# Kernel tuning notes

Hardware: AMD Instinct MI355X
Metric: run time of the kernel (lower is better)

## Reference

```python
import jax, jax.numpy as jnp
import numpy as np
from jax import lax

B, T, D_IN, H1, H2 = 200, 500, 300, 256, 300


def _lstm(x, Wih, Whh, bih, bhh, H):
    """PyTorch-convention LSTM (gate order i,f,g,o), zero init state.
    x: [B,T,Din] -> outputs [B,T,H]."""
    b = x.shape[0]
    # Precompute input contribution for all timesteps: [B,T,4H]
    xg = jnp.einsum('bti,gi->btg', x, Wih) + bih + bhh

    def step(carry, xg_t):
        h, c = carry
        g = xg_t + h @ Whh.T  # [B,4H]
        i = jax.nn.sigmoid(g[:, :H])
        f = jax.nn.sigmoid(g[:, H:2 * H])
        gg = jnp.tanh(g[:, 2 * H:3 * H])
        o = jax.nn.sigmoid(g[:, 3 * H:])
        c = f * c + i * gg
        h = o * jnp.tanh(c)
        return (h, c), h

    init = (jnp.zeros((b, H), x.dtype), jnp.zeros((b, H), x.dtype))
    _, hs = lax.scan(step, init, jnp.swapaxes(xg, 0, 1))  # [T,B,H]
    return jnp.swapaxes(hs, 0, 1)


def _uniform(key, shape, H):
    s = 1.0 / np.sqrt(H)
    return jax.random.uniform(key, shape, jnp.float32, -s, s)


def setup_inputs() -> dict:
    key = jax.random.key(0)
    ks = jax.random.split(key, 10)
    x = jax.random.normal(ks[0], (B, T, D_IN), jnp.float32)
    lengths = jax.random.randint(ks[1], (B,), 1, T + 1, jnp.int32)
    return {
        'x': x,
        'lengths': lengths,
        'Wih1': _uniform(ks[2], (4 * H1, D_IN), H1),
        'Whh1': _uniform(ks[3], (4 * H1, H1), H1),
        'bih1': _uniform(ks[4], (4 * H1,), H1),
        'bhh1': _uniform(ks[5], (4 * H1,), H1),
        'Wih2': _uniform(ks[6], (4 * H2, H1), H2),
        'Whh2': _uniform(ks[7], (4 * H2, H2), H2),
        'bih2': _uniform(ks[8], (4 * H2,), H2),
        'bhh2': _uniform(ks[9], (4 * H2,), H2),
    }


def reference(x, lengths, Wih1, Whh1, bih1, bhh1, Wih2, Whh2, bih2, bhh2):
    # lstm1 on packed sequence == causal per-sample LSTM + zero out padding
    out1 = _lstm(x, Wih1, Whh1, bih1, bhh1, H1)  # [B,T,H1]
    mask = (jnp.arange(T)[None, :] < lengths[:, None])  # [B,T]
    out1 = out1 * mask[:, :, None].astype(out1.dtype)   # pad_packed zeros
    # vectorized "last valid timestep" gather (replaces host-sync loop)
    idx = (lengths - 1).astype(jnp.int32)[:, None, None]
    h_value = jnp.take_along_axis(out1, idx, axis=1)[:, 0, :]  # [B,H1]
    # lstm2 runs over the full padded (zeroed) sequence, as in the original
    out2 = _lstm(out1, Wih2, Whh2, bih2, bhh2, H2)  # [B,T,H2]
    return (out2, h_value)
```

## Files before the change

### kernel.cpp

```cpp
#include <hip/hip_runtime.h>
#include <math.h>

#define TSEQ 500
#define BQ   200
#define DIN  300
#define H1   256
#define H2   300
#define K1   556
#define KP   576
#define H1P  256
#define H2P  304
#define BQC  25
#define LB1  8
#define LBT  18
#define NBLK 144

#define H1SLOT (BQ*H1P)
#define H2SLOT (BQ*H2P)

#define WS_H1   0
#define WS_H2   307200
#define WS_C1   672000
#define WS_C2   876800
#define WS_FLG  1132800
#define WS_MSET 1133824

#define POISON 0xFFFFFFFFFFFFFFFFull

typedef __attribute__((ext_vector_type(8))) short short8;
typedef __attribute__((ext_vector_type(4))) float f32x4;
typedef unsigned long long u64;

__device__ __forceinline__ float sigf(float v){ return 1.0f/(1.0f+__expf(-v)); }
__device__ __forceinline__ float tanhf_(float v){
    v = fminf(15.0f, fmaxf(-15.0f, v));
    float e = __expf(2.0f*v);
    return (e-1.0f)/(e+1.0f);
}
__device__ __forceinline__ unsigned short f2bf(float f){
    unsigned int xx = __builtin_bit_cast(unsigned int, f);
    xx = (xx + 0x7FFFu + ((xx>>16)&1u)) >> 16;
    return (unsigned short)xx;
}
__device__ __forceinline__ u64 ld8_sys(const void* p){
    return __hip_atomic_load((const u64*)p, __ATOMIC_RELAXED, __HIP_MEMORY_SCOPE_SYSTEM);
}
__device__ __forceinline__ void pub8(u64* p, u64 v){
    u64 old = __hip_atomic_exchange(p, v, __ATOMIC_RELAXED, __HIP_MEMORY_SCOPE_SYSTEM);
    asm volatile("" :: "v"(old));
}

union U16B { short8 s8; u64 u[2]; unsigned short us[8]; };
union U8B  { u64 u; unsigned short us[4]; };


__global__ __launch_bounds__(512, 2)
void lstm_mfma(const float* __restrict__ x, const int* __restrict__ lengths,
               const float* __restrict__ Wih1, const float* __restrict__ Whh1,
               const float* __restrict__ bih1, const float* __restrict__ bhh1,
               const float* __restrict__ Wih2, const float* __restrict__ Whh2,
               const float* __restrict__ bih2, const float* __restrict__ bhh2,
               float* __restrict__ out, char* __restrict__ wsb,
               int it_begin, int it_end, int coop)
{
    __shared__ unsigned short Al[32*KP];
    __shared__ float gl[128*33];
    __shared__ float bias[128];
    __shared__ int lenl[32];

    const int tid = threadIdx.x;
    const int bid = blockIdx.x;
    const int mc  = bid & 7;
    const int lbi = bid >> 3;
    const bool l1 = lbi < LB1;
    const int ub  = (l1 ? lbi : lbi - LB1) * 32;
    const int Hl  = l1 ? H1 : H2;

    unsigned short* h1s = (unsigned short*)(wsb + WS_H1);
    unsigned short* h2s = (unsigned short*)(wsb + WS_H2);
    float* c1 = (float*)(wsb + WS_C1);
    float* c2 = (float*)(wsb + WS_C2);
    int* flg = (int*)(wsb + WS_FLG + mc*128);

    const int wave = tid >> 6, lane = tid & 63;
    const int fr = lane & 15, fg = lane >> 4;
    const int sw = fr & 7;

    short8 wreg[18];
    {
        const int row = wave*16 + fr;
        const int u = row >> 2, g = row & 3;
        const int unit = ub + u;
        const bool vr = unit < Hl;
        const long grow = (long)g*Hl + unit;
        #pragma unroll
        for (int ks = 0; ks < 18; ++ks){
            unsigned short v8[8];
            #pragma unroll
            for (int j = 0; j < 8; ++j){
                int k = ks*32 + fg*8 + j;
                float v = 0.0f;
                if (vr && k < K1){
                    if (l1) v = (k < H1) ? Whh1[grow*H1 + k] : Wih1[grow*DIN + (k - H1)];
                    else    v = (k < H1) ? Wih2[grow*H1 + k] : Whh2[grow*H2 + (k - H1)];
                }
                v8[j] = f2bf(v);
            }
            wreg[ks] = *(short8*)v8;
        }
    }
    if (tid < 128){
        int u = tid >> 2, g = tid & 3, unit = ub + u;
        bias[tid] = (unit < Hl)
            ? ((l1?bih1:bih2)[g*Hl+unit] + (l1?bhh1:bhh2)[g*Hl+unit]) : 0.0f;
    }
    if (tid < 32) lenl[tid] = (tid < BQC) ? lengths[mc*BQC + tid] : 0;

    const unsigned short* arow0 = &Al[fr*KP];
    const unsigned short* arow1 = &Al[(16+fr)*KP];
    const int bg_e = mc*BQC + lane;
    const int unit4 = ub + wave*4;

    float creg[4] = {0.f, 0.f, 0.f, 0.f};
    if (!coop && lane < 32){
        float* cs = l1 ? c1 : c2;
        #pragma unroll
        for (int i2 = 0; i2 < 4; ++i2) creg[i2] = cs[(unit4 + i2)*BQ + bg_e];
    }

    __syncthreads();

    for (int it = it_begin; it < it_end; ++it){
        const bool active = l1 ? (it < TSEQ) : (it >= 1);
        const int t = l1 ? it : it - 1;

        if (l1){
            if (active){
                #pragma unroll
                for (int i = 0; i < 3; ++i){
                    int e = tid + i*512;
                    if (e < 1280){
                        int bl = e/40, kcx = 32 + e - (e/40)*40;
                        U16B v; v.u[0] = 0; v.u[1] = 0;
                        if (bl < BQC && kcx <= 69){
                            int bg = mc*BQC + bl;
                            const float* xp = x + ((size_t)bg*TSEQ + t)*DIN + (kcx*8 - 256);
                            float4 f0 = *(const float4*)xp;
                            v.us[0]=f2bf(f0.x); v.us[1]=f2bf(f0.y); v.us[2]=f2bf(f0.z); v.us[3]=f2bf(f0.w);
                            if (kcx <= 68){
                                float4 f1 = *(const float4*)(xp + 4);
                                v.us[4]=f2bf(f1.x); v.us[5]=f2bf(f1.y); v.us[6]=f2bf(f1.z); v.us[7]=f2bf(f1.w);
                            }
                        }
                        *(short8*)&Al[bl*KP + ((kcx ^ (bl&7))<<3)] = v.s8;
                    }
                }
                const unsigned short* h1p = h1s + (it%3)*H1SLOT;
                const int bl0 = tid>>5, kc0 = tid&31;
                const int bl1 = bl0 + 16;
                u64 a0=0, a1=0, a2=0, a3=0;
                const u64* p0 = (const u64*)(h1p + (size_t)(mc*BQC + bl0)*H1P + kc0*8);
                const u64* p2 = (const u64*)(h1p + (size_t)(mc*BQC + bl1)*H1P + kc0*8);
                const bool n0 = bl0 < BQC, n1 = bl1 < BQC;
                if (coop){
                    if (n0){ a0 = POISON; a1 = POISON; }
                    if (n1){ a2 = POISON; a3 = POISON; }
                    bool pend = n0 | n1;
                    while (pend){
                        if (a0 == POISON) a0 = ld8_sys(p0);
                        if (a1 == POISON) a1 = ld8_sys(p0 + 1);
                        if (a2 == POISON) a2 = ld8_sys(p2);
                        if (a3 == POISON) a3 = ld8_sys(p2 + 1);
                        pend = (a0==POISON)||(a1==POISON)||(a2==POISON)||(a3==POISON);
                        if (pend) __builtin_amdgcn_s_sleep(1);
                    }
                } else {
                    if (n0){ a0 = ld8_sys(p0); a1 = ld8_sys(p0 + 1); }
                    if (n1){ a2 = ld8_sys(p2); a3 = ld8_sys(p2 + 1); }
                }
                U16B w0; w0.u[0] = a0; w0.u[1] = a1;
                U16B w1; w1.u[0] = a2; w1.u[1] = a3;
                *(short8*)&Al[bl0*KP + ((kc0 ^ (bl0&7))<<3)] = w0.s8;
                *(short8*)&Al[bl1*KP + ((kc0 ^ (bl1&7))<<3)] = w1.s8;
            }
        } else {
            if (active){
                const unsigned short* h1p = h1s + (it%3)*H1SLOT;
                const unsigned short* h2p = h2s + ((it+2)%3)*H2SLOT;
                const u64* pp[5]; bool qa[5], qb[5]; u64 va[5], vb[5];
                #pragma unroll
                for (int i = 0; i < 5; ++i){
                    const int e = tid + i*512;
                    const int bl = e/72, kc = e - (e/72)*72;
                    pp[i] = nullptr; qa[i] = false; qb[i] = false; va[i] = 0; vb[i] = 0;
                    if (e < 2304 && bl < BQC && kc < 70){
                        const int bg = mc*BQC + bl;
                        if (kc < 32){
                            if (t < lenl[bl]){
                                pp[i] = (const u64*)(h1p + (size_t)bg*H1P + kc*8);
                                qa[i] = true; qb[i] = true;
                            }
                        } else {
                            pp[i] = (const u64*)(h2p + (size_t)bg*H2P + (kc*8 - 256));
                            qa[i] = true; qb[i] = (kc < 69);
                        }
                    }
                }
                if (coop){
                    #pragma unroll
                    for (int i = 0; i < 5; ++i){ if (qa[i]) va[i] = POISON; if (qb[i]) vb[i] = POISON; }
                    bool pend = true;
                    while (pend){
                        pend = false;
                        #pragma unroll
                        for (int i = 0; i < 5; ++i){
                            if (qa[i] && va[i] == POISON){ va[i] = ld8_sys(pp[i]);     pend |= (va[i] == POISON); }
                            if (qb[i] && vb[i] == POISON){ vb[i] = ld8_sys(pp[i] + 1); pend |= (vb[i] == POISON); }
                        }
                        if (pend) __builtin_amdgcn_s_sleep(1);
                    }
                } else {
                    #pragma unroll
                    for (int i = 0; i < 5; ++i){
                        if (qa[i]) va[i] = ld8_sys(pp[i]);
                        if (qb[i]) vb[i] = ld8_sys(pp[i] + 1);
                    }
                }
                #pragma unroll
                for (int i = 0; i < 5; ++i){
                    const int e = tid + i*512;
                    if (e < 2304){
                        const int bl = e/72, kc = e - (e/72)*72;
                        U16B v; v.u[0] = va[i]; v.u[1] = vb[i];
                        *(short8*)&Al[bl*KP + ((kc ^ (bl&7))<<3)] = v.s8;
                    }
                }
            }
        }

        __syncthreads();
        if (!l1 && coop && tid == 0)
            __hip_atomic_store(&flg[lbi], it + 1, __ATOMIC_RELAXED,
                               __HIP_MEMORY_SCOPE_SYSTEM);

        if (coop && lane < BQC){
            if (l1){
                if (it + 1 < TSEQ)
                    pub8((u64*)&h1s[((it+2)%3)*H1SLOT + (size_t)bg_e*H1P + unit4], POISON);
            } else if (unit4 < H2){
                pub8((u64*)&h2s[((it+1)%3)*H2SLOT + (size_t)bg_e*H2P + unit4], POISON);
            }
        }

        if (active){
            f32x4 acc0 = {0.f,0.f,0.f,0.f}, acc1 = {0.f,0.f,0.f,0.f};
            #pragma unroll
            for (int ks = 0; ks < 18; ++ks){
                const int off = ((ks*4 + fg) ^ sw) << 3;
                short8 b0 = *(const short8*)(arow0 + off);
                short8 b1 = *(const short8*)(arow1 + off);
                acc0 = __builtin_amdgcn_mfma_f32_16x16x32_bf16(wreg[ks], b0, acc0, 0, 0, 0);
                acc1 = __builtin_amdgcn_mfma_f32_16x16x32_bf16(wreg[ks], b1, acc1, 0, 0, 0);
            }
            const int gr = wave*16 + fg*4;
            #pragma unroll
            for (int q = 0; q < 4; ++q){
                gl[(gr+q)*33 + fr]      = acc0[q];
                gl[(gr+q)*33 + 16 + fr] = acc1[q];
            }
            if (lane < 32){
                float hv[4]; unsigned short hb[4];
                #pragma unroll
                for (int i2 = 0; i2 < 4; ++i2){
                    const int r = wave*16 + i2*4;
                    float gi = gl[(r+0)*33 + lane] + bias[r+0];
                    float gf = gl[(r+1)*33 + lane] + bias[r+1];
                    float gg = gl[(r+2)*33 + lane] + bias[r+2];
                    float go = gl[(r+3)*33 + lane] + bias[r+3];
                    float iv = sigf(gi), fv = sigf(gf), cv = tanhf_(gg), ov = sigf(go);
                    float c = fmaf(fv, creg[i2], iv*cv); creg[i2] = c;
                    hv[i2] = ov * tanhf_(c);
                    hb[i2] = f2bf(hv[i2]);
                }
                if (lane < BQC){
                    U8B pv; pv.us[0]=hb[0]; pv.us[1]=hb[1]; pv.us[2]=hb[2]; pv.us[3]=hb[3];
                    if (l1){
                        pub8((u64*)&h1s[((it+1)%3)*H1SLOT + (size_t)bg_e*H1P + unit4], pv.u);
                        if (it == lenl[lane] - 1){
                            float4 q; q.x=hv[0]; q.y=hv[1]; q.z=hv[2]; q.w=hv[3];
                            *(float4*)(out + 30000000 + (size_t)bg_e*H1 + unit4) = q;
                        }
                    } else if (unit4 < H2){
                        pub8((u64*)&h2s[(it%3)*H2SLOT + (size_t)bg_e*H2P + unit4], pv.u);
                        float4 q; q.x=hv[0]; q.y=hv[1]; q.z=hv[2]; q.w=hv[3];
                        *(float4*)(out + (size_t)bg_e*150000 + (size_t)t*300 + unit4) = q;
                    }
                }
            }
        }

        if (l1 && coop && (it + 1 < it_end) && tid < 10){
            while (__hip_atomic_load(&flg[8 + tid], __ATOMIC_RELAXED,
                                     __HIP_MEMORY_SCOPE_SYSTEM) < it + 1)
                __builtin_amdgcn_s_sleep(1);
        }

        asm volatile("s_waitcnt lgkmcnt(0)" ::: "memory");
        __builtin_amdgcn_sched_barrier(0);
        __builtin_amdgcn_s_barrier();
        __builtin_amdgcn_sched_barrier(0);
    }

    if (!coop && lane < 32){
        float* cs = l1 ? c1 : c2;
        #pragma unroll
        for (int i2 = 0; i2 < 4; ++i2) cs[(unit4 + i2)*BQ + bg_e] = creg[i2];
    }
}

extern "C" void kernel_launch(void* const* d_in, const int* in_sizes, int n_in,
                              void* d_out, int out_size, void* d_ws, size_t ws_size,
                              hipStream_t stream) {
    const float* x    = (const float*)d_in[0];
    const int*   lens = (const int*)  d_in[1];
    const float* Wih1 = (const float*)d_in[2];
    const float* Whh1 = (const float*)d_in[3];
    const float* bih1 = (const float*)d_in[4];
    const float* bhh1 = (const float*)d_in[5];
    const float* Wih2 = (const float*)d_in[6];
    const float* Whh2 = (const float*)d_in[7];
    const float* bih2 = (const float*)d_in[8];
    const float* bhh2 = (const float*)d_in[9];
    float* out = (float*)d_out;
    char*  ws  = (char*)d_ws;

    hipMemsetAsync(d_ws, 0, (size_t)WS_MSET, stream);
    hipMemsetAsync(ws + WS_H1 + H1SLOT*2 , 0xFF,
                   (size_t)H1SLOT*2, stream);

    int ib = 0, ie = TSEQ + 1, coop = 1;
    void* args[] = {(void*)&x, (void*)&lens, (void*)&Wih1, (void*)&Whh1, (void*)&bih1, (void*)&bhh1,
                    (void*)&Wih2, (void*)&Whh2, (void*)&bih2, (void*)&bhh2,
                    (void*)&out, (void*)&ws, (void*)&ib, (void*)&ie, (void*)&coop};
    hipError_t err = hipLaunchCooperativeKernel((const void*)lstm_mfma, dim3(NBLK), dim3(512),
                                                args, 0, stream);
    if (err != hipSuccess) {
        (void)hipGetLastError();
        for (int it = 0; it <= TSEQ; ++it) {
            hipLaunchKernelGGL(lstm_mfma, dim3(NBLK), dim3(512), 0, stream,
                               x, lens, Wih1, Whh1, bih1, bhh1, Wih2, Whh2, bih2, bhh2,
                               out, ws, it, it + 1, 0);
        }
    }
}
```

Before: 2.932 ms.

## Halve block count with 64 units per block and switch to per-wave flag synchronization

Each block now covers 64 hidden units with two weight row-tiles held in registers, so the grid shrinks from 144 to 72 blocks at one block per CU. The poison-value polling on hidden-state data is replaced by per-wave ready flags, written after a vmcnt wait, plus reader-done flags that layer 2 sets for layer 1. The aim is to cut cross-block handshake traffic and the repeated poisoning stores on every timestep. The cost is fewer CUs doing the recurrent work, about twice the MFMA work per block, and higher register pressure.

```diff
diff --git a/kernel.cpp b/kernel.cpp
--- a/kernel.cpp
+++ b/kernel.cpp
@@ -11,9 +11,10 @@
 #define H1P  256
 #define H2P  304
 #define BQC  25
-#define LB1  8
-#define LBT  18
-#define NBLK 144
+#define LB1  4
+#define LB2  5
+#define LBT  9
+#define NBLK 72
 
 #define H1SLOT (BQ*H1P)
 #define H2SLOT (BQ*H2P)
@@ -23,9 +24,7 @@
 #define WS_C1   672000
 #define WS_C2   876800
 #define WS_FLG  1132800
-#define WS_MSET 1133824
-
-#define POISON 0xFFFFFFFFFFFFFFFFull
+#define WS_MSET 1136896
 
 typedef __attribute__((ext_vector_type(8))) short short8;
 typedef __attribute__((ext_vector_type(4))) float f32x4;
@@ -49,12 +48,18 @@
     u64 old = __hip_atomic_exchange(p, v, __ATOMIC_RELAXED, __HIP_MEMORY_SCOPE_SYSTEM);
     asm volatile("" :: "v"(old));
 }
+__device__ __forceinline__ int ldflag(const int* p){
+    return __hip_atomic_load(p, __ATOMIC_RELAXED, __HIP_MEMORY_SCOPE_SYSTEM);
+}
+__device__ __forceinline__ void stflag(int* p, int v){
+    __hip_atomic_store(p, v, __ATOMIC_RELAXED, __HIP_MEMORY_SCOPE_SYSTEM);
+}
 
 union U16B { short8 s8; u64 u[2]; unsigned short us[8]; };
 union U8B  { u64 u; unsigned short us[4]; };
 
 
-__global__ __launch_bounds__(512, 2)
+__global__ __launch_bounds__(512, 1)
 void lstm_mfma(const float* __restrict__ x, const int* __restrict__ lengths,
                const float* __restrict__ Wih1, const float* __restrict__ Whh1,
                const float* __restrict__ bih1, const float* __restrict__ bhh1,
@@ -64,8 +69,8 @@
                int it_begin, int it_end, int coop)
 {
     __shared__ unsigned short Al[32*KP];
-    __shared__ float gl[128*33];
-    __shared__ float bias[128];
+    __shared__ float gl[256*33];
+    __shared__ float bias[256];
     __shared__ int lenl[32];
 
     const int tid = threadIdx.x;
@@ -73,22 +78,24 @@
     const int mc  = bid & 7;
     const int lbi = bid >> 3;
     const bool l1 = lbi < LB1;
-    const int ub  = (l1 ? lbi : lbi - LB1) * 32;
+    const int ub  = (l1 ? lbi : lbi - LB1) * 64;
     const int Hl  = l1 ? H1 : H2;
 
     unsigned short* h1s = (unsigned short*)(wsb + WS_H1);
     unsigned short* h2s = (unsigned short*)(wsb + WS_H2);
     float* c1 = (float*)(wsb + WS_C1);
     float* c2 = (float*)(wsb + WS_C2);
-    int* flg = (int*)(wsb + WS_FLG + mc*128);
+    int* wflg  = (int*)(wsb + WS_FLG + mc*512);
+    int* rdflg = wflg + 80;
 
     const int wave = tid >> 6, lane = tid & 63;
     const int fr = lane & 15, fg = lane >> 4;
     const int sw = fr & 7;
 
-    short8 wreg[18];
-    {
-        const int row = wave*16 + fr;
+    short8 wreg[2][18];
+    #pragma unroll
+    for (int rt = 0; rt < 2; ++rt){
+        const int row = wave*32 + rt*16 + fr;
         const int u = row >> 2, g = row & 3;
         const int unit = ub + u;
         const bool vr = unit < Hl;
@@ -106,10 +113,10 @@
                 }
                 v8[j] = f2bf(v);
             }
-            wreg[ks] = *(short8*)v8;
-        }
-    }
-    if (tid < 128){
+            wreg[rt][ks] = *(short8*)v8;
+        }
+    }
+    if (tid < 256){
         int u = tid >> 2, g = tid & 3, unit = ub + u;
         bias[tid] = (unit < Hl)
             ? ((l1?bih1:bih2)[g*Hl+unit] + (l1?bhh1:bhh2)[g*Hl+unit]) : 0.0f;
@@ -119,13 +126,13 @@
     const unsigned short* arow0 = &Al[fr*KP];
     const unsigned short* arow1 = &Al[(16+fr)*KP];
     const int bg_e = mc*BQC + lane;
-    const int unit4 = ub + wave*4;
-
-    float creg[4] = {0.f, 0.f, 0.f, 0.f};
-    if (!coop && lane < 32){
+    const int unit8 = ub + wave*8;
+
+    float creg[8] = {0.f,0.f,0.f,0.f,0.f,0.f,0.f,0.f};
+    if (!coop && lane < BQC){
         float* cs = l1 ? c1 : c2;
         #pragma unroll
-        for (int i2 = 0; i2 < 4; ++i2) creg[i2] = cs[(unit4 + i2)*BQ + bg_e];
+        for (int j = 0; j < 8; ++j) creg[j] = cs[(unit8 + j)*BQ + bg_e];
     }
 
     __syncthreads();
@@ -134,8 +141,8 @@
         const bool active = l1 ? (it < TSEQ) : (it >= 1);
         const int t = l1 ? it : it - 1;
 
-        if (l1){
-            if (active){
+        if (active){
+            if (l1){
                 #pragma unroll
                 for (int i = 0; i < 3; ++i){
                     int e = tid + i*512;
@@ -155,76 +162,68 @@
                         *(short8*)&Al[bl*KP + ((kcx ^ (bl&7))<<3)] = v.s8;
                     }
                 }
+                const int kc0 = tid & 31;
+                if (coop && it > it_begin){
+                    const int* fp = wflg + kc0;
+                    while (ldflag(fp) < it) __builtin_amdgcn_s_sleep(1);
+                    asm volatile("" ::: "memory");
+                }
                 const unsigned short* h1p = h1s + (it%3)*H1SLOT;
-                const int bl0 = tid>>5, kc0 = tid&31;
-                const int bl1 = bl0 + 16;
+                const int bl0 = tid >> 5, bl1 = bl0 + 16;
                 u64 a0=0, a1=0, a2=0, a3=0;
-                const u64* p0 = (const u64*)(h1p + (size_t)(mc*BQC + bl0)*H1P + kc0*8);
-                const u64* p2 = (const u64*)(h1p + (size_t)(mc*BQC + bl1)*H1P + kc0*8);
-                const bool n0 = bl0 < BQC, n1 = bl1 < BQC;
-                if (coop){
-                    if (n0){ a0 = POISON; a1 = POISON; }
-                    if (n1){ a2 = POISON; a3 = POISON; }
-                    bool pend = n0 | n1;
-                    while (pend){
-                        if (a0 == POISON) a0 = ld8_sys(p0);
-                        if (a1 == POISON) a1 = ld8_sys(p0 + 1);
-                        if (a2 == POISON) a2 = ld8_sys(p2);
-                        if (a3 == POISON) a3 = ld8_sys(p2 + 1);
-                        pend = (a0==POISON)||(a1==POISON)||(a2==POISON)||(a3==POISON);
-                        if (pend) __builtin_amdgcn_s_sleep(1);
-                    }
-                } else {
-                    if (n0){ a0 = ld8_sys(p0); a1 = ld8_sys(p0 + 1); }
-                    if (n1){ a2 = ld8_sys(p2); a3 = ld8_sys(p2 + 1); }
+                {
+                    const u64* p0 = (const u64*)(h1p + (size_t)(mc*BQC + bl0)*H1P + kc0*8);
+                    a0 = ld8_sys(p0); a1 = ld8_sys(p0 + 1);
+                }
+                if (bl1 < BQC){
+                    const u64* p2 = (const u64*)(h1p + (size_t)(mc*BQC + bl1)*H1P + kc0*8);
+                    a2 = ld8_sys(p2); a3 = ld8_sys(p2 + 1);
                 }
                 U16B w0; w0.u[0] = a0; w0.u[1] = a1;
                 U16B w1; w1.u[0] = a2; w1.u[1] = a3;
                 *(short8*)&Al[bl0*KP + ((kc0 ^ (bl0&7))<<3)] = w0.s8;
                 *(short8*)&Al[bl1*KP + ((kc0 ^ (bl1&7))<<3)] = w1.s8;
-            }
-        } else {
-            if (active){
+            } else {
                 const unsigned short* h1p = h1s + (it%3)*H1SLOT;
                 const unsigned short* h2p = h2s + ((it+2)%3)*H2SLOT;
-                const u64* pp[5]; bool qa[5], qb[5]; u64 va[5], vb[5];
+                const u64* pp[5]; bool qa[5], qb[5], fq[5]; const int* fpp[5];
+                u64 va[5], vb[5];
                 #pragma unroll
                 for (int i = 0; i < 5; ++i){
                     const int e = tid + i*512;
                     const int bl = e/72, kc = e - (e/72)*72;
-                    pp[i] = nullptr; qa[i] = false; qb[i] = false; va[i] = 0; vb[i] = 0;
+                    pp[i] = nullptr; fpp[i] = wflg; qa[i]=false; qb[i]=false; fq[i]=false;
+                    va[i] = 0; vb[i] = 0;
                     if (e < 2304 && bl < BQC && kc < 70){
                         const int bg = mc*BQC + bl;
                         if (kc < 32){
                             if (t < lenl[bl]){
                                 pp[i] = (const u64*)(h1p + (size_t)bg*H1P + kc*8);
-                                qa[i] = true; qb[i] = true;
+                                qa[i] = true; qb[i] = true; fq[i] = true; fpp[i] = wflg + kc;
                             }
                         } else {
                             pp[i] = (const u64*)(h2p + (size_t)bg*H2P + (kc*8 - 256));
-                            qa[i] = true; qb[i] = (kc < 69);
+                            qa[i] = true; qb[i] = (kc < 69); fq[i] = true; fpp[i] = wflg + kc;
                         }
                     }
                 }
                 if (coop){
-                    #pragma unroll
-                    for (int i = 0; i < 5; ++i){ if (qa[i]) va[i] = POISON; if (qb[i]) vb[i] = POISON; }
-                    bool pend = true;
+                    bool pend = fq[0]|fq[1]|fq[2]|fq[3]|fq[4];
                     while (pend){
                         pend = false;
                         #pragma unroll
-                        for (int i = 0; i < 5; ++i){
-                            if (qa[i] && va[i] == POISON){ va[i] = ld8_sys(pp[i]);     pend |= (va[i] == POISON); }
-                            if (qb[i] && vb[i] == POISON){ vb[i] = ld8_sys(pp[i] + 1); pend |= (vb[i] == POISON); }
-                        }
+                        for (int i = 0; i < 5; ++i)
+                            if (fq[i]){
+                                if (ldflag(fpp[i]) >= it) fq[i] = false; else pend = true;
+                            }
                         if (pend) __builtin_amdgcn_s_sleep(1);
                     }
-                } else {
-                    #pragma unroll
-                    for (int i = 0; i < 5; ++i){
-                        if (qa[i]) va[i] = ld8_sys(pp[i]);
-                        if (qb[i]) vb[i] = ld8_sys(pp[i] + 1);
-                    }
+                    asm volatile("" ::: "memory");
+                }
+                #pragma unroll
+                for (int i = 0; i < 5; ++i){
+                    if (qa[i]) va[i] = ld8_sys(pp[i]);
+                    if (qb[i]) vb[i] = ld8_sys(pp[i] + 1);
                 }
                 #pragma unroll
                 for (int i = 0; i < 5; ++i){
@@ -237,84 +236,92 @@
                 }
             }
         }
-
         __syncthreads();
         if (!l1 && coop && tid == 0)
-            __hip_atomic_store(&flg[lbi], it + 1, __ATOMIC_RELAXED,
-                               __HIP_MEMORY_SCOPE_SYSTEM);
-
-        if (coop && lane < BQC){
-            if (l1){
-                if (it + 1 < TSEQ)
-                    pub8((u64*)&h1s[((it+2)%3)*H1SLOT + (size_t)bg_e*H1P + unit4], POISON);
-            } else if (unit4 < H2){
-                pub8((u64*)&h2s[((it+1)%3)*H2SLOT + (size_t)bg_e*H2P + unit4], POISON);
-            }
-        }
+            stflag(&rdflg[lbi - LB1], it + 1);
 
         if (active){
-            f32x4 acc0 = {0.f,0.f,0.f,0.f}, acc1 = {0.f,0.f,0.f,0.f};
+            f32x4 a00={0.f,0.f,0.f,0.f}, a01={0.f,0.f,0.f,0.f};
+            f32x4 a10={0.f,0.f,0.f,0.f}, a11={0.f,0.f,0.f,0.f};
             #pragma unroll
             for (int ks = 0; ks < 18; ++ks){
                 const int off = ((ks*4 + fg) ^ sw) << 3;
                 short8 b0 = *(const short8*)(arow0 + off);
                 short8 b1 = *(const short8*)(arow1 + off);
-                acc0 = __builtin_amdgcn_mfma_f32_16x16x32_bf16(wreg[ks], b0, acc0, 0, 0, 0);
-                acc1 = __builtin_amdgcn_mfma_f32_16x16x32_bf16(wreg[ks], b1, acc1, 0, 0, 0);
-            }
-            const int gr = wave*16 + fg*4;
+                a00 = __builtin_amdgcn_mfma_f32_16x16x32_bf16(wreg[0][ks], b0, a00, 0, 0, 0);
+                a01 = __builtin_amdgcn_mfma_f32_16x16x32_bf16(wreg[0][ks], b1, a01, 0, 0, 0);
+                a10 = __builtin_amdgcn_mfma_f32_16x16x32_bf16(wreg[1][ks], b0, a10, 0, 0, 0);
+                a11 = __builtin_amdgcn_mfma_f32_16x16x32_bf16(wreg[1][ks], b1, a11, 0, 0, 0);
+            }
+            const int r0 = wave*32 + fg*4;
             #pragma unroll
             for (int q = 0; q < 4; ++q){
-                gl[(gr+q)*33 + fr]      = acc0[q];
-                gl[(gr+q)*33 + 16 + fr] = acc1[q];
-            }
-            if (lane < 32){
-                float hv[4]; unsigned short hb[4];
-                #pragma unroll
-                for (int i2 = 0; i2 < 4; ++i2){
-                    const int r = wave*16 + i2*4;
+                gl[(r0+q)*33 + fr]         = a00[q];
+                gl[(r0+q)*33 + 16 + fr]    = a01[q];
+                gl[(r0+16+q)*33 + fr]      = a10[q];
+                gl[(r0+16+q)*33 + 16 + fr] = a11[q];
+            }
+            if (lane < BQC){
+                float hv[8]; unsigned short hb[8];
+                #pragma unroll
+                for (int j = 0; j < 8; ++j){
+                    const int r = wave*32 + 4*j;
                     float gi = gl[(r+0)*33 + lane] + bias[r+0];
                     float gf = gl[(r+1)*33 + lane] + bias[r+1];
                     float gg = gl[(r+2)*33 + lane] + bias[r+2];
                     float go = gl[(r+3)*33 + lane] + bias[r+3];
                     float iv = sigf(gi), fv = sigf(gf), cv = tanhf_(gg), ov = sigf(go);
-                    float c = fmaf(fv, creg[i2], iv*cv); creg[i2] = c;
-                    hv[i2] = ov * tanhf_(c);
-                    hb[i2] = f2bf(hv[i2]);
-                }
-                if (lane < BQC){
-                    U8B pv; pv.us[0]=hb[0]; pv.us[1]=hb[1]; pv.us[2]=hb[2]; pv.us[3]=hb[3];
-                    if (l1){
-                        pub8((u64*)&h1s[((it+1)%3)*H1SLOT + (size_t)bg_e*H1P + unit4], pv.u);
-                        if (it == lenl[lane] - 1){
-                            float4 q; q.x=hv[0]; q.y=hv[1]; q.z=hv[2]; q.w=hv[3];
-                            *(float4*)(out + 30000000 + (size_t)bg_e*H1 + unit4) = q;
+                    float c = fmaf(fv, creg[j], iv*cv); creg[j] = c;
+                    hv[j] = ov * tanhf_(c);
+                    hb[j] = f2bf(hv[j]);
+                }
+                U8B p0, p1;
+                p0.us[0]=hb[0]; p0.us[1]=hb[1]; p0.us[2]=hb[2]; p0.us[3]=hb[3];
+                p1.us[0]=hb[4]; p1.us[1]=hb[5]; p1.us[2]=hb[6]; p1.us[3]=hb[7];
+                if (l1){
+                    u64* dp = (u64*)&h1s[((it+1)%3)*H1SLOT + (size_t)bg_e*H1P + unit8];
+                    pub8(dp, p0.u); pub8(dp + 1, p1.u);
+                    if (it == lenl[lane] - 1){
+                        float* hp = out + 30000000 + (size_t)bg_e*H1 + unit8;
+                        float4 q0; q0.x=hv[0]; q0.y=hv[1]; q0.z=hv[2]; q0.w=hv[3];
+                        float4 q1; q1.x=hv[4]; q1.y=hv[5]; q1.z=hv[6]; q1.w=hv[7];
+                        *(float4*)hp = q0; *(float4*)(hp + 4) = q1;
+                    }
+                } else {
+                    u64* dp = (u64*)&h2s[(it%3)*H2SLOT + (size_t)bg_e*H2P + unit8];
+                    if (unit8 < H2)     pub8(dp, p0.u);
+                    if (unit8 + 4 < H2) pub8(dp + 1, p1.u);
+                    if (unit8 < H2){
+                        float* op = out + (size_t)bg_e*150000 + (size_t)t*300 + unit8;
+                        float4 q0; q0.x=hv[0]; q0.y=hv[1]; q0.z=hv[2]; q0.w=hv[3];
+                        *(float4*)op = q0;
+                        if (unit8 + 4 < H2){
+                            float4 q1; q1.x=hv[4]; q1.y=hv[5]; q1.z=hv[6]; q1.w=hv[7];
+                            *(float4*)(op + 4) = q1;
                         }
-                    } else if (unit4 < H2){
-                        pub8((u64*)&h2s[(it%3)*H2SLOT + (size_t)bg_e*H2P + unit4], pv.u);
-                        float4 q; q.x=hv[0]; q.y=hv[1]; q.z=hv[2]; q.w=hv[3];
-                        *(float4*)(out + (size_t)bg_e*150000 + (size_t)t*300 + unit4) = q;
-                    }
-                }
-            }
-        }
-
-        if (l1 && coop && (it + 1 < it_end) && tid < 10){
-            while (__hip_atomic_load(&flg[8 + tid], __ATOMIC_RELAXED,
-                                     __HIP_MEMORY_SCOPE_SYSTEM) < it + 1)
-                __builtin_amdgcn_s_sleep(1);
-        }
-
+                    }
+                }
+            }
+        }
+
+        if (coop){
+            asm volatile("s_waitcnt vmcnt(0)" ::: "memory");
+            __builtin_amdgcn_sched_barrier(0);
+            if (lane == 0) stflag(&wflg[lbi*8 + wave], it + 1);
+        }
+        if (l1 && coop && it > 0 && it < TSEQ-1 && tid < LB2){
+            while (ldflag(&rdflg[tid]) < it) __builtin_amdgcn_s_sleep(1);
+        }
         asm volatile("s_waitcnt lgkmcnt(0)" ::: "memory");
         __builtin_amdgcn_sched_barrier(0);
         __builtin_amdgcn_s_barrier();
         __builtin_amdgcn_sched_barrier(0);
     }
 
-    if (!coop && lane < 32){
+    if (!coop && lane < BQC){
         float* cs = l1 ? c1 : c2;
         #pragma unroll
-        for (int i2 = 0; i2 < 4; ++i2) cs[(unit4 + i2)*BQ + bg_e] = creg[i2];
+        for (int j = 0; j < 8; ++j) cs[(unit8 + j)*BQ + bg_e] = creg[j];
     }
 }
 
@@ -335,8 +342,6 @@
     char*  ws  = (char*)d_ws;
 
     hipMemsetAsync(d_ws, 0, (size_t)WS_MSET, stream);
-    hipMemsetAsync(ws + WS_H1 + H1SLOT*2 , 0xFF,
-                   (size_t)H1SLOT*2, stream);
 
     int ib = 0, ie = TSEQ + 1, coop = 1;
     void* args[] = {(void*)&x, (void*)&lens, (void*)&Wih1, (void*)&Whh1, (void*)&bih1, (void*)&bhh1,
```

Result: slower. 5.623 ms (+91.8%).
